# Kernel tuning notes

Hardware: AMD Instinct MI355X
Metric: run time of the kernel (lower is better)

## Reference

```python
import jax, jax.numpy as jnp
import numpy as np

N_NODES = 165888   # 2048 puzzles * 81 cells
N_EDGES = 3317760  # 2048 * 1620 directed sudoku-constraint edges
HID = 64
N_LAYERS = 4
LN_EPS = 1e-5


def setup_inputs() -> dict:
    key = jax.random.key(0)
    ks = jax.random.split(key, 16)
    x = jax.random.normal(ks[0], (N_NODES, 9), dtype=jnp.float32)
    edge_index = jax.random.randint(ks[1], (2, N_EDGES), 0, N_NODES, dtype=jnp.int64)
    s = 0.1
    return {
        "x": x,
        "edge_index": edge_index,
        "W_in": jax.random.normal(ks[2], (HID, 9), dtype=jnp.float32) * s,
        "b_in": jnp.zeros((HID,), jnp.float32),
        "W_rel": jax.random.normal(ks[3], (N_LAYERS, HID, HID), dtype=jnp.float32) * s,
        "W_root": jax.random.normal(ks[4], (N_LAYERS, HID, HID), dtype=jnp.float32) * s,
        "b_conv": jnp.zeros((N_LAYERS, HID), jnp.float32),
        "W_res": jax.random.normal(ks[5], (HID, HID), dtype=jnp.float32) * s,
        "b_res": jnp.zeros((HID,), jnp.float32),
        "ln_g": jnp.ones((HID,), jnp.float32),
        "ln_b": jnp.zeros((HID,), jnp.float32),
        "W_out": jax.random.normal(ks[6], (9, HID), dtype=jnp.float32) * s,
        "b_out": jnp.zeros((9,), jnp.float32),
    }


def _layer_norm(h, g, b):
    mu = jnp.mean(h, axis=-1, keepdims=True)
    var = jnp.mean(jnp.square(h - mu), axis=-1, keepdims=True)
    return (h - mu) * jax.lax.rsqrt(var + LN_EPS) * g + b


def reference(x, edge_index, W_in, b_in, W_rel, W_root, b_conv, W_res, b_res,
              ln_g, ln_b, W_out, b_out):
    # input projection: [N, 9] -> [N, HID]
    h = x @ W_in.T + b_in
    residual = h @ W_res.T + b_res  # computed once before the conv stack
    src, dst = edge_index[0], edge_index[1]
    n = h.shape[0]
    for l in range(N_LAYERS):
        # GraphConv (PyG semantics, aggr='add'): gather neighbor feats, scatter-add to dst
        agg = jax.ops.segment_sum(h[src], dst, num_segments=n)
        h = h @ W_root[l].T + agg @ W_rel[l].T + b_conv[l]
        h = _layer_norm(h, ln_g, ln_b)
        h = jnp.where(h > 0, h, 0.01 * h)  # leaky_relu(0.01); dropout = identity (eval)
        h = h + residual
    out = h @ W_out.T + b_out  # [N, 9]
    return out.reshape(-1, 9, 9, 9)
```

## Files before the change

### kernel.cpp

```cpp
#include <hip/hip_runtime.h>

#define N_NODES 165888
#define N_EDGES 3317760
#define NBKT 648
#define NB 512
#define EPB (N_EDGES / NB)
#define HSZ (NBKT * NB)
#define LN_EPS 1e-5f

typedef _Float16 f16;
typedef _Float16 half8 __attribute__((ext_vector_type(8)));
typedef float f32x4 __attribute__((ext_vector_type(4)));

__device__ __forceinline__ f32x4 mfma16(half8 a, half8 b, f32x4 c) {
    return __builtin_amdgcn_mfma_f32_16x16x32_f16(a, b, c, 0, 0, 0);
}


__global__ __launch_bounds__(256) void k_hist2d(const int* __restrict__ dst,
                                                int* __restrict__ h2) {
    __shared__ int hist[NBKT];
    int t = threadIdx.x, b = blockIdx.x;
    for (int i = t; i < NBKT; i += 256) hist[i] = 0;
    __syncthreads();
    int e0 = b * EPB;
    for (int e = e0 + t; e < e0 + EPB; e += 256)
        atomicAdd(&hist[dst[e] >> 8], 1);
    __syncthreads();
    for (int i = t; i < NBKT; i += 256)
        h2[i * NB + b] = hist[i];
}

__global__ void k_scan1(int* __restrict__ h2, int* __restrict__ bsum) {
    __shared__ int s[1024];
    int t = threadIdx.x;
    int i = blockIdx.x * 1024 + t;
    int own = h2[i];
    s[t] = own;
    __syncthreads();
    for (int off = 1; off < 1024; off <<= 1) {
        int u = (t >= off) ? s[t - off] : 0;
        __syncthreads();
        s[t] += u;
        __syncthreads();
    }
    h2[i] = s[t] - own;
    if (t == 1023) bsum[blockIdx.x] = s[1023];
}

__global__ void k_scan2(const int* __restrict__ bsum, int* __restrict__ bsumx,
                        int* __restrict__ h2) {
    __shared__ int s[512];
    int t = threadIdx.x;
    int v = (t < HSZ / 1024) ? bsum[t] : 0;
    s[t] = v;
    __syncthreads();
    for (int off = 1; off < 512; off <<= 1) {
        int u = (t >= off) ? s[t - off] : 0;
        __syncthreads();
        s[t] += u;
        __syncthreads();
    }
    if (t < HSZ / 1024) bsumx[t] = s[t] - v;
    if (t == 0) h2[HSZ] = N_EDGES;
}

__global__ void k_scan3(int* __restrict__ h2, const int* __restrict__ bsumx) {
    int i = blockIdx.x * 1024 + threadIdx.x;
    h2[i] += bsumx[blockIdx.x];
}

__global__ __launch_bounds__(256) void k_scatter(const int* __restrict__ src,
                                                 const int* __restrict__ dst,
                                                 const int* __restrict__ h2,
                                                 unsigned* __restrict__ pairs) {
    __shared__ int cur[NBKT];
    int t = threadIdx.x, b = blockIdx.x;
    for (int i = t; i < NBKT; i += 256) cur[i] = h2[i * NB + b];
    __syncthreads();
    int e0 = b * EPB;
    for (int e = e0 + t; e < e0 + EPB; e += 256) {
        int d = dst[e];
        int pos = atomicAdd(&cur[d >> 8], 1);
        pairs[pos] = ((unsigned)(d & 255) << 24) | (unsigned)src[e];
    }
}

__global__ __launch_bounds__(256) void k_csr(const unsigned* __restrict__ pairs,
                                             const int* __restrict__ h2,
                                             int* __restrict__ roff,
                                             int* __restrict__ csr) {
    __shared__ int hist[256];
    __shared__ int sc[256];
    __shared__ int curs[256];
    int b = blockIdx.x;
    int e0 = h2[b * NB], e1 = h2[(b + 1) * NB];
    int t = threadIdx.x;
    hist[t] = 0;
    __syncthreads();
    for (int p = e0 + t; p < e1; p += 256)
        atomicAdd(&hist[pairs[p] >> 24], 1);
    __syncthreads();
    int own = hist[t];
    sc[t] = own;
    __syncthreads();
    for (int off = 1; off < 256; off <<= 1) {
        int u = (t >= off) ? sc[t - off] : 0;
        __syncthreads();
        sc[t] += u;
        __syncthreads();
    }
    int base = e0 + sc[t] - own;
    roff[(b << 8) + t] = base;
    curs[t] = base;
    if (b == 0 && t == 0) roff[N_NODES] = N_EDGES;
    __syncthreads();
    for (int p = e0 + t; p < e1; p += 256) {
        unsigned pk = pairs[p];
        int pos = atomicAdd(&curs[pk >> 24], 1);
        csr[pos] = (int)(pk & 0xFFFFFF);
    }
}


__global__ void k_wcvt(const float* __restrict__ Wroot, const float* __restrict__ Wrel,
                       const float* __restrict__ Wres, const float* __restrict__ Win,
                       f16* __restrict__ W2h, f16* __restrict__ Wresh, f16* __restrict__ Winh) {
    int i = blockIdx.x * 256 + threadIdx.x;
    if (i < 4 * 64 * 128) {
        int l = i >> 13, r = i & 8191, j = r >> 7, k = r & 127;
        float v = (k < 64) ? Wroot[l * 4096 + j * 64 + k] : Wrel[l * 4096 + j * 64 + k - 64];
        W2h[i] = (f16)v;
    } else if (i < 4 * 64 * 128 + 4096) {
        int t = i - 4 * 64 * 128;
        Wresh[t] = (f16)Wres[t];
    } else if (i < 4 * 64 * 128 + 4096 + 2048) {
        int t = i - (4 * 64 * 128 + 4096);
        int j = t >> 5, k = t & 31;
        Winh[t] = (k < 9) ? (f16)Win[j * 9 + k] : (f16)0.f;
    }
}


__global__ __launch_bounds__(256) void k_proj(
        const float* __restrict__ x, const f16* __restrict__ Winh,
        const float* __restrict__ bin, const f16* __restrict__ Wresh,
        const float* __restrict__ bres, f16* __restrict__ h0,
        f16* __restrict__ res) {
    __shared__ f16 hs[4][16][64];
    int tid = threadIdx.x, w = tid >> 6, lane = tid & 63, li = lane & 15, kg = lane >> 4;
    int nb = blockIdx.x * 64 + w * 16;
    int node = nb + li;

    half8 ax;
    #pragma unroll
    for (int e = 0; e < 8; ++e) ax[e] = (f16)0.f;
    if (kg == 0) {
        #pragma unroll
        for (int e = 0; e < 8; ++e) ax[e] = (f16)x[(size_t)node * 9 + e];
    } else if (kg == 1) {
        ax[0] = (f16)x[(size_t)node * 9 + 8];
    }

    f32x4 ch[4];
    #pragma unroll
    for (int jt = 0; jt < 4; ++jt) {
        half8 b = *(const half8*)(Winh + (jt * 16 + li) * 32 + kg * 8);
        f32x4 z = {0.f, 0.f, 0.f, 0.f};
        ch[jt] = mfma16(ax, b, z);
    }
    #pragma unroll
    for (int jt = 0; jt < 4; ++jt) {
        float bb = bin[jt * 16 + li];
        #pragma unroll
        for (int r = 0; r < 4; ++r) {
            int row = kg * 4 + r;
            float v = ch[jt][r] + bb;
            f16 hv = (f16)v;
            h0[(size_t)(nb + row) * 64 + jt * 16 + li] = hv;
            int col = jt * 16 + li;
            hs[w][row][col ^ ((row & 7) * 8)] = hv;
        }
    }
    __syncthreads();

    f32x4 cr[4];
    #pragma unroll
    for (int jt = 0; jt < 4; ++jt) { f32x4 z = {0.f,0.f,0.f,0.f}; cr[jt] = z; }
    #pragma unroll
    for (int s = 0; s < 2; ++s) {
        int k0 = s * 32 + kg * 8;
        half8 a = *(const half8*)(&hs[w][li][k0 ^ ((li & 7) * 8)]);
        #pragma unroll
        for (int jt = 0; jt < 4; ++jt) {
            half8 b = *(const half8*)(Wresh + (jt * 16 + li) * 64 + k0);
            cr[jt] = mfma16(a, b, cr[jt]);
        }
    }
    #pragma unroll
    for (int jt = 0; jt < 4; ++jt) {
        float bb = bres[jt * 16 + li];
        #pragma unroll
        for (int r = 0; r < 4; ++r)
            res[(size_t)(nb + kg * 4 + r) * 64 + jt * 16 + li] = (f16)(cr[jt][r] + bb);
    }
}


__global__ __launch_bounds__(256) void k_layer(
        const f16* __restrict__ h, const f16* __restrict__ res,
        const int* __restrict__ roff, const int* __restrict__ csr,
        const f16* __restrict__ W2h, const float* __restrict__ bconv,
        const float* __restrict__ lng, const float* __restrict__ lnb,
        f16* __restrict__ hn) {
    __shared__ f16 hs[4][16][64];
    int tid = threadIdx.x, lane = tid & 63, w = tid >> 6;
    int g = lane >> 3, s = lane & 7;
    int blk = blockIdx.x;

    #pragma unroll
    for (int r2 = 0; r2 < 2; ++r2) {
        int nl = r2 * 8 + g;
        int n = blk * 64 + w * 16 + nl;
        int e0 = roff[n], e1 = roff[n + 1];
        float a[8];
        #pragma unroll
        for (int j = 0; j < 8; ++j) a[j] = 0.f;

        int p = e0;
        for (; p + 7 < e1; p += 8) {
            half8 v[8];
            #pragma unroll
            for (int q = 0; q < 8; ++q) {
                int idx = csr[p + q];
                v[q] = *(const half8*)(h + ((size_t)idx << 6) + s * 8);
            }
            #pragma unroll
            for (int q = 0; q < 8; ++q) {
                #pragma unroll
                for (int j = 0; j < 8; ++j) a[j] += (float)v[q][j];
            }
        }
        for (; p + 3 < e1; p += 4) {
            half8 v[4];
            #pragma unroll
            for (int q = 0; q < 4; ++q) {
                int idx = csr[p + q];
                v[q] = *(const half8*)(h + ((size_t)idx << 6) + s * 8);
            }
            #pragma unroll
            for (int q = 0; q < 4; ++q) {
                #pragma unroll
                for (int j = 0; j < 8; ++j) a[j] += (float)v[q][j];
            }
        }
        for (; p < e1; ++p) {
            int idx = csr[p];
            half8 v0 = *(const half8*)(h + ((size_t)idx << 6) + s * 8);
            #pragma unroll
            for (int j = 0; j < 8; ++j) a[j] += (float)v0[j];
        }

        half8 o;
        #pragma unroll
        for (int j = 0; j < 8; ++j) o[j] = (f16)a[j];
        *(half8*)(&hs[w][nl][(s ^ (nl & 7)) * 8]) = o;
    }

    int li = lane & 15, kg = lane >> 4;
    int nb = blk * 64 + w * 16;
    int node = nb + li;

    f32x4 C[4];
    #pragma unroll
    for (int jt = 0; jt < 4; ++jt) { f32x4 z = {0.f,0.f,0.f,0.f}; C[jt] = z; }

    #pragma unroll
    for (int st = 0; st < 4; ++st) {
        half8 a;
        if (st < 2) {
            a = *(const half8*)(h + ((size_t)node << 6) + st * 32 + kg * 8);
        } else {
            int m = (st - 2) * 4 + kg;
            a = *(const half8*)(&hs[w][li][(m ^ (li & 7)) * 8]);
        }
        #pragma unroll
        for (int jt = 0; jt < 4; ++jt) {
            half8 b = *(const half8*)(W2h + (size_t)(jt * 16 + li) * 128 + st * 32 + kg * 8);
            C[jt] = mfma16(a, b, C[jt]);
        }
    }

    #pragma unroll
    for (int jt = 0; jt < 4; ++jt) {
        float bb = bconv[jt * 16 + li];
        #pragma unroll
        for (int r = 0; r < 4; ++r) C[jt][r] += bb;
    }

    float mu[4], rstd[4];
    #pragma unroll
    for (int r = 0; r < 4; ++r) {
        float v = C[0][r] + C[1][r] + C[2][r] + C[3][r];
        v += __shfl_xor(v, 1, 64); v += __shfl_xor(v, 2, 64);
        v += __shfl_xor(v, 4, 64); v += __shfl_xor(v, 8, 64);
        mu[r] = v * (1.f / 64.f);
    }
    #pragma unroll
    for (int r = 0; r < 4; ++r) {
        float d0 = C[0][r] - mu[r], d1 = C[1][r] - mu[r];
        float d2 = C[2][r] - mu[r], d3 = C[3][r] - mu[r];
        float vv = d0 * d0 + d1 * d1 + d2 * d2 + d3 * d3;
        vv += __shfl_xor(vv, 1, 64); vv += __shfl_xor(vv, 2, 64);
        vv += __shfl_xor(vv, 4, 64); vv += __shfl_xor(vv, 8, 64);
        rstd[r] = rsqrtf(vv * (1.f / 64.f) + LN_EPS);
    }
    #pragma unroll
    for (int jt = 0; jt < 4; ++jt) {
        float gg = lng[jt * 16 + li], bb = lnb[jt * 16 + li];
        #pragma unroll
        for (int r = 0; r < 4; ++r) {
            size_t idx = (size_t)(nb + kg * 4 + r) * 64 + jt * 16 + li;
            float y = (C[jt][r] - mu[r]) * rstd[r] * gg + bb;
            y = (y > 0.f) ? y : 0.01f * y;
            y += (float)res[idx];
            hn[idx] = (f16)y;
        }
    }
}


__global__ __launch_bounds__(256) void k_out(
        const f16* __restrict__ h, const float* __restrict__ Wout,
        const float* __restrict__ bout, float* __restrict__ out) {
    int node = blockIdx.x * 256 + threadIdx.x;
    float acc[9];
    #pragma unroll
    for (int c = 0; c < 9; ++c) acc[c] = bout[c];
    #pragma unroll
    for (int cc = 0; cc < 8; ++cc) {
        half8 v = *(const half8*)(h + ((size_t)node << 6) + cc * 8);
        float f[8];
        #pragma unroll
        for (int e = 0; e < 8; ++e) f[e] = (float)v[e];
        #pragma unroll
        for (int c = 0; c < 9; ++c) {
            #pragma unroll
            for (int e = 0; e < 8; ++e)
                acc[c] += f[e] * Wout[c * 64 + cc * 8 + e];
        }
    }
    #pragma unroll
    for (int c = 0; c < 9; ++c) out[(size_t)node * 9 + c] = acc[c];
}

extern "C" void kernel_launch(void* const* d_in, const int* in_sizes, int n_in,
                              void* d_out, int out_size, void* d_ws, size_t ws_size,
                              hipStream_t stream) {
    const float* x     = (const float*)d_in[0];
    const int*   ei    = (const int*)d_in[1];
    const float* Win   = (const float*)d_in[2];
    const float* bin   = (const float*)d_in[3];
    const float* Wrel  = (const float*)d_in[4];
    const float* Wroot = (const float*)d_in[5];
    const float* bconv = (const float*)d_in[6];
    const float* Wres  = (const float*)d_in[7];
    const float* bres  = (const float*)d_in[8];
    const float* lng   = (const float*)d_in[9];
    const float* lnb   = (const float*)d_in[10];
    const float* Wout  = (const float*)d_in[11];
    const float* bout  = (const float*)d_in[12];
    float* out = (float*)d_out;

    char* p = (char*)d_ws;
    auto alloc = [&](size_t bytes) {
        char* r = p;
        p += (bytes + 255) & ~(size_t)255;
        return r;
    };
    f16*      h0    = (f16*)alloc((size_t)N_NODES * 64 * 2);
    f16*      h1    = (f16*)alloc((size_t)N_NODES * 64 * 2);
    f16*      res   = (f16*)alloc((size_t)N_NODES * 64 * 2);
    unsigned* pairs = (unsigned*)alloc((size_t)N_EDGES * 4);
    int*      csr   = (int*)alloc((size_t)N_EDGES * 4);
    int*      roff  = (int*)alloc((size_t)(N_NODES + 1) * 4);
    int*      h2    = (int*)alloc((size_t)(HSZ + 1) * 4);
    int*      bsum  = (int*)alloc((HSZ / 1024) * 4);
    int*      bsumx = (int*)alloc((HSZ / 1024) * 4);
    f16*      W2h   = (f16*)alloc(4 * 64 * 128 * 2);
    f16*      Wresh = (f16*)alloc(64 * 64 * 2);
    f16*      Winh  = (f16*)alloc(64 * 32 * 2);

    const int* srcv = ei;
    const int* dstv = ei + N_EDGES;

    k_hist2d<<<NB, 256, 0, stream>>>(dstv, h2);
    k_scan1<<<HSZ / 1024, 1024, 0, stream>>>(h2, bsum);
    k_scan2<<<1, 512, 0, stream>>>(bsum, bsumx, h2);
    k_scan3<<<HSZ / 1024, 1024, 0, stream>>>(h2, bsumx);
    k_scatter<<<NB, 256, 0, stream>>>(srcv, dstv, h2, pairs);
    k_csr<<<NBKT, 256, 0, stream>>>(pairs, h2, roff, csr);

    k_wcvt<<<152, 256, 0, stream>>>(Wroot, Wrel, Wres, Win, W2h, Wresh, Winh);
    k_proj<<<N_NODES / 64, 256, 0, stream>>>(x, Winh, bin, Wresh, bres, h0, res);

    f16* ha = h0;
    f16* hb = h1;
    for (int l = 0; l < 4; ++l) {
        k_layer<<<N_NODES / 64, 256, 0, stream>>>(ha, res, roff, csr,
                                                  W2h + (size_t)l * 64 * 128,
                                                  bconv + l * 64, lng, lnb, hb);
        f16* t = ha; ha = hb; hb = t;
    }
    k_out<<<N_NODES / 256, 256, 0, stream>>>(ha, Wout, bout, out);
}
```

Measured before the change: 443.7 us.

## Sub-sort CSR neighbors by source range to improve gather locality

The CSR build now buckets each destination's neighbor list into eight source-index ranges and stores the per-range counts, packed as 8-bit fields, in a new 64-bit array. The layer kernel walks these ranges in order for the two nodes each lane group handles, so that concurrent gathers tend to touch the same slice of the feature array and hit cache more often. In exchange the gather loop is split into many short per-range loops with 4-way instead of 8-way unrolling, which reduces the number of loads in flight. Each per-range count must also stay below 256 or it overflows its packed field.

Result: slower. 689.7 us (+55.4%).

```diff
diff --git a/kernel.cpp b/kernel.cpp
--- a/kernel.cpp
+++ b/kernel.cpp
@@ -6,11 +6,13 @@
 #define NB 512
 #define EPB (N_EDGES / NB)
 #define HSZ (NBKT * NB)
+#define RNG 20736
 #define LN_EPS 1e-5f
 
 typedef _Float16 f16;
 typedef _Float16 half8 __attribute__((ext_vector_type(8)));
 typedef float f32x4 __attribute__((ext_vector_type(4)));
+typedef unsigned long long u64;
 
 __device__ __forceinline__ f32x4 mfma16(half8 a, half8 b, f32x4 c) {
     return __builtin_amdgcn_mfma_f32_16x16x32_f16(a, b, c, 0, 0, 0);
@@ -89,36 +91,53 @@
 __global__ __launch_bounds__(256) void k_csr(const unsigned* __restrict__ pairs,
                                              const int* __restrict__ h2,
                                              int* __restrict__ roff,
+                                             u64* __restrict__ roffpk,
                                              int* __restrict__ csr) {
-    __shared__ int hist[256];
-    __shared__ int sc[256];
-    __shared__ int curs[256];
+    __shared__ int hist[2048];
+    __shared__ int tsum[256];
     int b = blockIdx.x;
     int e0 = h2[b * NB], e1 = h2[(b + 1) * NB];
     int t = threadIdx.x;
-    hist[t] = 0;
-    __syncthreads();
-    for (int p = e0 + t; p < e1; p += 256)
-        atomicAdd(&hist[pairs[p] >> 24], 1);
-    __syncthreads();
-    int own = hist[t];
-    sc[t] = own;
-    __syncthreads();
-    for (int off = 1; off < 256; off <<= 1) {
-        int u = (t >= off) ? sc[t - off] : 0;
-        __syncthreads();
-        sc[t] += u;
-        __syncthreads();
-    }
-    int base = e0 + sc[t] - own;
-    roff[(b << 8) + t] = base;
-    curs[t] = base;
-    if (b == 0 && t == 0) roff[N_NODES] = N_EDGES;
+    for (int i = t; i < 2048; i += 256) hist[i] = 0;
     __syncthreads();
     for (int p = e0 + t; p < e1; p += 256) {
         unsigned pk = pairs[p];
-        int pos = atomicAdd(&curs[pk >> 24], 1);
-        csr[pos] = (int)(pk & 0xFFFFFF);
+        int sv = (int)(pk & 0xFFFFFF);
+        int key = (int)((pk >> 24) << 3) | (sv / RNG);
+        atomicAdd(&hist[key], 1);
+    }
+    __syncthreads();
+    int c[8];
+    int sum = 0;
+    u64 pkc = 0;
+    #pragma unroll
+    for (int r = 0; r < 8; ++r) {
+        c[r] = hist[t * 8 + r];
+        pkc |= (u64)(unsigned)c[r] << (8 * r);
+        sum += c[r];
+    }
+    roffpk[(b << 8) + t] = pkc;
+    tsum[t] = sum;
+    __syncthreads();
+    for (int off = 1; off < 256; off <<= 1) {
+        int u = (t >= off) ? tsum[t - off] : 0;
+        __syncthreads();
+        tsum[t] += u;
+        __syncthreads();
+    }
+    int base = e0 + tsum[t] - sum;
+    roff[(b << 8) + t] = base;
+    if (b == 0 && t == 0) roff[N_NODES] = N_EDGES;
+    int run = base;
+    #pragma unroll
+    for (int r = 0; r < 8; ++r) { int cc = c[r]; hist[t * 8 + r] = run; run += cc; }
+    __syncthreads();
+    for (int p = e0 + t; p < e1; p += 256) {
+        unsigned pk = pairs[p];
+        int sv = (int)(pk & 0xFFFFFF);
+        int key = (int)((pk >> 24) << 3) | (sv / RNG);
+        int pos = atomicAdd(&hist[key], 1);
+        csr[pos] = sv;
     }
 }
 
@@ -209,7 +228,8 @@
 
 __global__ __launch_bounds__(256) void k_layer(
         const f16* __restrict__ h, const f16* __restrict__ res,
-        const int* __restrict__ roff, const int* __restrict__ csr,
+        const int* __restrict__ roff, const u64* __restrict__ roffpk,
+        const int* __restrict__ csr,
         const f16* __restrict__ W2h, const float* __restrict__ bconv,
         const float* __restrict__ lng, const float* __restrict__ lnb,
         f16* __restrict__ hn) {
@@ -218,58 +238,57 @@
     int g = lane >> 3, s = lane & 7;
     int blk = blockIdx.x;
 
-    #pragma unroll
-    for (int r2 = 0; r2 < 2; ++r2) {
-        int nl = r2 * 8 + g;
-        int n = blk * 64 + w * 16 + nl;
-        int e0 = roff[n], e1 = roff[n + 1];
-        float a[8];
-        #pragma unroll
-        for (int j = 0; j < 8; ++j) a[j] = 0.f;
-
-        int p = e0;
-        for (; p + 7 < e1; p += 8) {
-            half8 v[8];
+    int nb16 = blk * 64 + w * 16;
+    int n0 = nb16 + g, n1 = nb16 + 8 + g;
+    int cur0 = roff[n0], cur1 = roff[n1];
+    u64 pk0 = roffpk[n0], pk1 = roffpk[n1];
+
+    float A0[8], A1[8];
+    #pragma unroll
+    for (int j = 0; j < 8; ++j) { A0[j] = 0.f; A1[j] = 0.f; }
+
+    for (int r = 0; r < 8; ++r) {
+        int c0 = (int)((pk0 >> (8 * r)) & 255);
+        int c1 = (int)((pk1 >> (8 * r)) & 255);
+        int end0 = cur0 + c0, end1 = cur1 + c1;
+        for (; cur0 + 3 < end0; cur0 += 4) {
+            half8 v0 = *(const half8*)(h + ((size_t)csr[cur0]     << 6) + s * 8);
+            half8 v1 = *(const half8*)(h + ((size_t)csr[cur0 + 1] << 6) + s * 8);
+            half8 v2 = *(const half8*)(h + ((size_t)csr[cur0 + 2] << 6) + s * 8);
+            half8 v3 = *(const half8*)(h + ((size_t)csr[cur0 + 3] << 6) + s * 8);
             #pragma unroll
-            for (int q = 0; q < 8; ++q) {
-                int idx = csr[p + q];
-                v[q] = *(const half8*)(h + ((size_t)idx << 6) + s * 8);
-            }
+            for (int j = 0; j < 8; ++j)
+                A0[j] += ((float)v0[j] + (float)v1[j]) + ((float)v2[j] + (float)v3[j]);
+        }
+        for (; cur0 < end0; ++cur0) {
+            half8 v0 = *(const half8*)(h + ((size_t)csr[cur0] << 6) + s * 8);
             #pragma unroll
-            for (int q = 0; q < 8; ++q) {
-                #pragma unroll
-                for (int j = 0; j < 8; ++j) a[j] += (float)v[q][j];
-            }
-        }
-        for (; p + 3 < e1; p += 4) {
-            half8 v[4];
+            for (int j = 0; j < 8; ++j) A0[j] += (float)v0[j];
+        }
+        for (; cur1 + 3 < end1; cur1 += 4) {
+            half8 v0 = *(const half8*)(h + ((size_t)csr[cur1]     << 6) + s * 8);
+            half8 v1 = *(const half8*)(h + ((size_t)csr[cur1 + 1] << 6) + s * 8);
+            half8 v2 = *(const half8*)(h + ((size_t)csr[cur1 + 2] << 6) + s * 8);
+            half8 v3 = *(const half8*)(h + ((size_t)csr[cur1 + 3] << 6) + s * 8);
             #pragma unroll
-            for (int q = 0; q < 4; ++q) {
-                int idx = csr[p + q];
-                v[q] = *(const half8*)(h + ((size_t)idx << 6) + s * 8);
-            }
+            for (int j = 0; j < 8; ++j)
+                A1[j] += ((float)v0[j] + (float)v1[j]) + ((float)v2[j] + (float)v3[j]);
+        }
+        for (; cur1 < end1; ++cur1) {
+            half8 v0 = *(const half8*)(h + ((size_t)csr[cur1] << 6) + s * 8);
             #pragma unroll
-            for (int q = 0; q < 4; ++q) {
-                #pragma unroll
-                for (int j = 0; j < 8; ++j) a[j] += (float)v[q][j];
-            }
-        }
-        for (; p < e1; ++p) {
-            int idx = csr[p];
-            half8 v0 = *(const half8*)(h + ((size_t)idx << 6) + s * 8);
-            #pragma unroll
-            for (int j = 0; j < 8; ++j) a[j] += (float)v0[j];
-        }
-
-        half8 o;
-        #pragma unroll
-        for (int j = 0; j < 8; ++j) o[j] = (f16)a[j];
-        *(half8*)(&hs[w][nl][(s ^ (nl & 7)) * 8]) = o;
-    }
+            for (int j = 0; j < 8; ++j) A1[j] += (float)v0[j];
+        }
+    }
+
+    half8 o0, o1;
+    #pragma unroll
+    for (int j = 0; j < 8; ++j) { o0[j] = (f16)A0[j]; o1[j] = (f16)A1[j]; }
+    *(half8*)(&hs[w][g][(s ^ (g & 7)) * 8]) = o0;
+    *(half8*)(&hs[w][8 + g][(s ^ (g & 7)) * 8]) = o1;
 
     int li = lane & 15, kg = lane >> 4;
-    int nb = blk * 64 + w * 16;
-    int node = nb + li;
+    int node = nb16 + li;
 
     f32x4 C[4];
     #pragma unroll
@@ -320,7 +339,7 @@
         float gg = lng[jt * 16 + li], bb = lnb[jt * 16 + li];
         #pragma unroll
         for (int r = 0; r < 4; ++r) {
-            size_t idx = (size_t)(nb + kg * 4 + r) * 64 + jt * 16 + li;
+            size_t idx = (size_t)(nb16 + kg * 4 + r) * 64 + jt * 16 + li;
             float y = (C[jt][r] - mu[r]) * rstd[r] * gg + bb;
             y = (y > 0.f) ? y : 0.01f * y;
             y += (float)res[idx];
@@ -378,18 +397,19 @@
         p += (bytes + 255) & ~(size_t)255;
         return r;
     };
-    f16*      h0    = (f16*)alloc((size_t)N_NODES * 64 * 2);
-    f16*      h1    = (f16*)alloc((size_t)N_NODES * 64 * 2);
-    f16*      res   = (f16*)alloc((size_t)N_NODES * 64 * 2);
-    unsigned* pairs = (unsigned*)alloc((size_t)N_EDGES * 4);
-    int*      csr   = (int*)alloc((size_t)N_EDGES * 4);
-    int*      roff  = (int*)alloc((size_t)(N_NODES + 1) * 4);
-    int*      h2    = (int*)alloc((size_t)(HSZ + 1) * 4);
-    int*      bsum  = (int*)alloc((HSZ / 1024) * 4);
-    int*      bsumx = (int*)alloc((HSZ / 1024) * 4);
-    f16*      W2h   = (f16*)alloc(4 * 64 * 128 * 2);
-    f16*      Wresh = (f16*)alloc(64 * 64 * 2);
-    f16*      Winh  = (f16*)alloc(64 * 32 * 2);
+    f16*      h0     = (f16*)alloc((size_t)N_NODES * 64 * 2);
+    f16*      h1     = (f16*)alloc((size_t)N_NODES * 64 * 2);
+    f16*      res    = (f16*)alloc((size_t)N_NODES * 64 * 2);
+    unsigned* pairs  = (unsigned*)alloc((size_t)N_EDGES * 4);
+    int*      csr    = (int*)alloc((size_t)N_EDGES * 4);
+    int*      roff   = (int*)alloc((size_t)(N_NODES + 1) * 4);
+    u64*      roffpk = (u64*)alloc((size_t)N_NODES * 8);
+    int*      h2     = (int*)alloc((size_t)(HSZ + 1) * 4);
+    int*      bsum   = (int*)alloc((HSZ / 1024) * 4);
+    int*      bsumx  = (int*)alloc((HSZ / 1024) * 4);
+    f16*      W2h    = (f16*)alloc(4 * 64 * 128 * 2);
+    f16*      Wresh  = (f16*)alloc(64 * 64 * 2);
+    f16*      Winh   = (f16*)alloc(64 * 32 * 2);
 
     const int* srcv = ei;
     const int* dstv = ei + N_EDGES;
@@ -399,7 +419,7 @@
     k_scan2<<<1, 512, 0, stream>>>(bsum, bsumx, h2);
     k_scan3<<<HSZ / 1024, 1024, 0, stream>>>(h2, bsumx);
     k_scatter<<<NB, 256, 0, stream>>>(srcv, dstv, h2, pairs);
-    k_csr<<<NBKT, 256, 0, stream>>>(pairs, h2, roff, csr);
+    k_csr<<<NBKT, 256, 0, stream>>>(pairs, h2, roff, roffpk, csr);
 
     k_wcvt<<<152, 256, 0, stream>>>(Wroot, Wrel, Wres, Win, W2h, Wresh, Winh);
     k_proj<<<N_NODES / 64, 256, 0, stream>>>(x, Winh, bin, Wresh, bres, h0, res);
@@ -407,7 +427,7 @@
     f16* ha = h0;
     f16* hb = h1;
     for (int l = 0; l < 4; ++l) {
-        k_layer<<<N_NODES / 64, 256, 0, stream>>>(ha, res, roff, csr,
+        k_layer<<<N_NODES / 64, 256, 0, stream>>>(ha, res, roff, roffpk, csr,
                                                   W2h + (size_t)l * 64 * 128,
                                                   bconv + l * 64, lng, lnb, hb);
         f16* t = ha; ha = hb; hb = t;
```
